# Kernel optimization log

Hardware: AMD Instinct MI355X
Metric: run time of the kernel (lower is better)

## Reference

```python
import jax, jax.numpy as jnp
import numpy as np


def setup_inputs() -> dict:
    key = jax.random.key(0)
    ks = jax.random.split(key, 7)
    T, B, X, H = 256, 64, 512, 2048
    s_ih = 1.0 / np.sqrt(H)
    return {
        "input": jax.random.normal(ks[0], (T, B, X), dtype=jnp.float32),
        "h_0": jax.random.normal(ks[1], (B, H), dtype=jnp.float32),
        "c_0": jax.random.normal(ks[2], (B, H), dtype=jnp.float32),
        "w_ih": jax.random.normal(ks[3], (4 * H, X), dtype=jnp.float32) * s_ih,
        "w_hh": jax.random.normal(ks[4], (4 * H, H), dtype=jnp.float32) * s_ih,
        "b_ih": jax.random.normal(ks[5], (4 * H,), dtype=jnp.float32) * s_ih,
        "b_hh": jax.random.normal(ks[6], (4 * H,), dtype=jnp.float32) * s_ih,
    }


def reference(input, h_0, c_0, w_ih, w_hh, b_ih, b_hh):
    H = h_0.shape[-1]
    # Precompute input projections for all timesteps in one big GEMM: [T,B,4H]
    x_proj = jnp.einsum("tbx,gx->tbg", input, w_ih) + b_ih + b_hh

    def step(carry, xg):
        h, c = carry
        gates = xg + h @ w_hh.T  # [B, 4H]
        i, f, g, o = jnp.split(gates, 4, axis=-1)  # torch LSTMCell gate order
        i = jax.nn.sigmoid(i)
        f = jax.nn.sigmoid(f)
        g = jnp.tanh(g)
        o = jax.nn.sigmoid(o)
        c_new = f * c + i * g
        h_new = o * jnp.tanh(c_new)
        y = jax.nn.softmax(h_new, axis=-1)  # per-step softmax over hidden dim
        return (h_new, c_new), y

    (h_T, c_T), ys = jax.lax.scan(step, (h_0, c_0), x_proj)
    return ys, h_T, c_T
```

## Files before the change

kernel.cpp:

```cpp
#include <hip/hip_runtime.h>

#define Tn 256
#define Bn 64
#define Xn 512
#define Hn 2048
#define Gn 8192
#define NWG 256

typedef short bf16x8 __attribute__((ext_vector_type(8)));
typedef float f32x4 __attribute__((ext_vector_type(4)));
typedef unsigned uint32x4 __attribute__((ext_vector_type(4)));

#define AL(p)    __hip_atomic_load((p), __ATOMIC_RELAXED, __HIP_MEMORY_SCOPE_AGENT)
#define AS(p, v) __hip_atomic_store((p), (v), __ATOMIC_RELAXED, __HIP_MEMORY_SCOPE_AGENT)

static __device__ __forceinline__ unsigned short f2bf(float f) {
    unsigned int u = __builtin_bit_cast(unsigned int, f);
    u += 0x7fffu + ((u >> 16) & 1u);
    return (unsigned short)(u >> 16);
}
static __device__ __forceinline__ float bf2f(unsigned short s) {
    unsigned int u = ((unsigned int)s) << 16;
    return __builtin_bit_cast(float, u);
}
static __device__ __forceinline__ void cvt4(const float* __restrict__ s,
                                            unsigned short* __restrict__ d, int i) {
    float4 v = ((const float4*)s)[i];
    ushort4 o;
    o.x = f2bf(v.x); o.y = f2bf(v.y); o.z = f2bf(v.z); o.w = f2bf(v.w);
    ((ushort4*)d)[i] = o;
}
static __device__ __forceinline__ float sigm(float x) {
    return 1.f / (1.f + __expf(-x));
}
static __device__ __forceinline__ float ftanh(float x) {
    float e = __expf(2.f * x);
    return (e - 1.f) / (e + 1.f);
}

template <int RING>
static __device__ __forceinline__ size_t hoff(int t) {
    if constexpr (RING) return (size_t)((t * 97) % 257) * 262144;
    else                return (size_t)(t & 1) * 262144;
}

template <int RING>
static __device__ __forceinline__ bf16x8 ldh(const unsigned short* p) {
    if constexpr (RING) {
        return *(const bf16x8*)p;
    } else {
        unsigned* q = (unsigned*)p;
        uint32x4 v;
        v[0] = AL(q + 0); v[1] = AL(q + 1); v[2] = AL(q + 2); v[3] = AL(q + 3);
        return __builtin_bit_cast(bf16x8, v);
    }
}
template <int RING>
static __device__ __forceinline__ float ldh1(const unsigned short* hb, int idx) {
    if constexpr (RING) {
        return bf2f(hb[idx]);
    } else {
        unsigned d = AL((unsigned*)(hb + (idx & ~1)));
        return bf2f((idx & 1) ? (unsigned short)(d >> 16) : (unsigned short)(d & 0xffffu));
    }
}

static __device__ __forceinline__ void flags_wait(unsigned* flags, unsigned t, int l) {
    if (!t) return;
    unsigned* p = flags + l * 4;
    for (;;) {
        unsigned a0 = AL(p + 0), a1 = AL(p + 1), a2 = AL(p + 2), a3 = AL(p + 3);
        bool ok = (a0 >= t) & (a1 >= t) & (a2 >= t) & (a3 >= t);
        if (__all(ok)) break;
        __builtin_amdgcn_s_sleep(1);
    }
}

__global__ void prologue3(const float* __restrict__ x, const float* __restrict__ h0,
                          const float* __restrict__ b_ih, const float* __restrict__ b_hh,
                          const float* __restrict__ w_ih,
                          unsigned short* __restrict__ Xb, unsigned short* __restrict__ XFrag,
                          unsigned short* __restrict__ hb0, float* __restrict__ bias,
                          unsigned* __restrict__ flags)
{
    int i = blockIdx.x * blockDim.x + threadIdx.x;
    const int n_x  = Tn * Bn * Xn / 4;
    const int n_xf = Gn * Xn / 4;
    const int n_h  = Bn * Hn / 4;
    const int n_b  = Gn / 4;
    if (i < n_x) { cvt4(x, Xb, i); return; }
    i -= n_x;
    if (i < n_xf) {
        int wg = i >> 12, r = i & 4095;
        int c = r >> 7, k = (r & 127) * 4;
        int g = c >> 3, u = c & 7;
        float4 v = *(const float4*)(w_ih + (size_t)(g * Hn + wg * 8 + u) * Xn + k);
        ushort4 o;
        o.x = f2bf(v.x); o.y = f2bf(v.y); o.z = f2bf(v.z); o.w = f2bf(v.w);
        int ct = c >> 4, kk = k >> 5, l = ((k >> 3) & 3) * 16 + (c & 15);
        *(ushort4*)((char*)XFrag + (size_t)wg * 32768 + (size_t)((ct * 16 + kk) * 64 + l) * 16 + (k & 7) * 2) = o;
        return;
    }
    i -= n_xf;
    if (i < n_h) {
        int flat = i * 4;
        int row = flat >> 11, unit0 = flat & 2047;
        float4 v = ((const float4*)h0)[i];
        ushort4 o;
        o.x = f2bf(v.x); o.y = f2bf(v.y); o.z = f2bf(v.z); o.w = f2bf(v.w);
        int dst = (((unit0 >> 3) << 6) + row) * 8 + (unit0 & 7);
        *(ushort4*)(hb0 + dst) = o;
        return;
    }
    i -= n_h;
    if (i < n_b) {
        float4 a = ((const float4*)b_ih)[i];
        float4 b = ((const float4*)b_hh)[i];
        ((float4*)bias)[i] = make_float4(a.x + b.x, a.y + b.y, a.z + b.z, a.w + b.w);
        return;
    }
    i -= n_b;
    if (i < 256) flags[i] = 0u;
}

#define MFMA2() \
    acc0 = __builtin_amdgcn_mfma_f32_16x16x32_bf16(a, b0, acc0, 0, 0, 0); \
    acc1 = __builtin_amdgcn_mfma_f32_16x16x32_bf16(a, b1, acc1, 0, 0, 0);

template <int RING>
__global__ __launch_bounds__(512, 1) void lstm_persist3(
    const unsigned short* __restrict__ Xb, const unsigned short* __restrict__ XFrag,
    const float* __restrict__ bias, const float* __restrict__ c0,
    char* __restrict__ hbase, const float* __restrict__ w_hh,
    float* __restrict__ ys, float* __restrict__ hT, float* __restrict__ cT,
    unsigned* __restrict__ flags)
{
    extern __shared__ char smem[];
    const unsigned short* LW = (const unsigned short*)smem;
    float* RED  = (float*)(smem + 131072);
    float* RED2 = (float*)(smem + 139264);

    const int wg  = blockIdx.x;
    const int tid = threadIdx.x;
    const int U0  = wg * 8;

    for (int i = tid; i < 32 * 512; i += 512) {
        int c = i >> 9, k = (i & 511) * 4;
        int g = c >> 3, u = c & 7;
        float4 v = *(const float4*)(w_hh + (size_t)(g * Hn + U0 + u) * Hn + k);
        ushort4 o;
        o.x = f2bf(v.x); o.y = f2bf(v.y); o.z = f2bf(v.z); o.w = f2bf(v.w);
        int ct = c >> 4, kk = k >> 5, l = ((k >> 3) & 3) * 16 + (c & 15);
        *(ushort4*)(smem + ((size_t)((ct * 64 + kk) * 64 + l) * 16 + (k & 7) * 2)) = o;
    }
    __syncthreads();

    const int w = tid >> 6, l = tid & 63;
    const int lm = l & 15, lh = l >> 4;
    const int kh = w >> 2, rblk = w & 3, rb = rblk * 16;
    const int kk0 = kh * 32;
    const int kx0 = kh * 8;

    const int u  = lm & 7;
    const bool hi = (lm & 8) != 0;
    const int r0g = rb + 4 * lh + (hi ? 2 : 0);

    float bi = 0.f, bf_ = 0.f, bg = 0.f, bo = 0.f, cs0 = 0.f, cs1 = 0.f;
    if (kh == 0) {
        bi  = bias[0 * Hn + U0 + u];
        bf_ = bias[1 * Hn + U0 + u];
        bg  = bias[2 * Hn + U0 + u];
        bo  = bias[3 * Hn + U0 + u];
        cs0 = c0[(size_t)r0g * Hn + U0 + u];
        cs1 = c0[(size_t)(r0g + 1) * Hn + U0 + u];
    }

    const char* xfb = (const char*)XFrag + (size_t)wg * 32768;

    for (int t = 0; t < Tn; ++t) {
        const unsigned short* hb = (const unsigned short*)(hbase + hoff<RING>(t));
        unsigned short* hn = (unsigned short*)(hbase + hoff<RING>(t + 1));

        f32x4 acc0 = {0.f, 0.f, 0.f, 0.f}, acc1 = {0.f, 0.f, 0.f, 0.f};

        {
            const unsigned short* xa = Xb + (size_t)(t * 64 + rb + lm) * Xn + lh * 8;
            bf16x8 aP[4];
            #pragma unroll
            for (int j = 0; j < 4; ++j) aP[j] = *(const bf16x8*)(xa + (kx0 + j) * 32);
            #pragma unroll 4
            for (int kkl = 0; kkl < 8; ++kkl) {
                bf16x8 a = aP[kkl & 3];
                if (kkl < 4) aP[kkl & 3] = *(const bf16x8*)(xa + (kx0 + kkl + 4) * 32);
                bf16x8 b0 = *(const bf16x8*)(xfb + ((size_t)((0 * 16 + kx0 + kkl) * 64 + l) << 4));
                bf16x8 b1 = *(const bf16x8*)(xfb + ((size_t)((1 * 16 + kx0 + kkl) * 64 + l) << 4));
                MFMA2();
            }
        }

        if (w == 0) flags_wait(flags, (unsigned)t, l);
        __syncthreads();

        {
            const unsigned short* ha = hb + (size_t)(rb + lm) * 8;
            bf16x8 aP[8];
            #pragma unroll
            for (int j = 0; j < 8; ++j)
                aP[j] = ldh<RING>(ha + (size_t)((kk0 + j) * 4 + lh) * 512);
            #pragma unroll 8
            for (int kkl = 0; kkl < 32; ++kkl) {
                bf16x8 a = aP[kkl & 7];
                if (kkl < 24)
                    aP[kkl & 7] = ldh<RING>(ha + (size_t)((kk0 + kkl + 8) * 4 + lh) * 512);
                bf16x8 b0 = *(const bf16x8*)(LW + ((size_t)((0 * 64 + kk0 + kkl) * 64 + l) << 3));
                bf16x8 b1 = *(const bf16x8*)(LW + ((size_t)((1 * 64 + kk0 + kkl) * 64 + l) << 3));
                MFMA2();
            }
        }

        const bool do_sm = (kh == 1) && (wg < Bn) && (t > 0);
        float sv[8];
        if (kh == 1) {
            int idx = (rblk * 64 + l) * 8;
            *(f32x4*)(RED + idx)     = acc0;
            *(f32x4*)(RED + idx + 4) = acc1;
            if (do_sm) {
                int row = wg;
                float m = -1e30f;
                #pragma unroll
                for (int j = 0; j < 8; ++j) {
                    int uu = rblk * 512 + j * 64 + l;
                    sv[j] = ldh1<RING>(hb, (uu >> 3) * 512 + row * 8 + (uu & 7));
                    m = fmaxf(m, sv[j]);
                }
                #pragma unroll
                for (int off = 32; off; off >>= 1) m = fmaxf(m, __shfl_xor(m, off));
                float s = 0.f;
                #pragma unroll
                for (int j = 0; j < 8; ++j) s += __expf(sv[j] - m);
                #pragma unroll
                for (int off = 32; off; off >>= 1) s += __shfl_xor(s, off);
                if (l == 0) { RED2[rblk * 2] = m; RED2[rblk * 2 + 1] = s; }
            }
        }
        __syncthreads();

        if (kh == 0) {
            int idx = (rblk * 64 + l) * 8;
            acc0 += *(const f32x4*)(RED + idx);
            acc1 += *(const f32x4*)(RED + idx + 4);
            f32x4 s0, s1;
            #pragma unroll
            for (int r = 0; r < 4; ++r) { s0[r] = __shfl_xor(acc0[r], 8); s1[r] = __shfl_xor(acc1[r], 8); }
            #pragma unroll
            for (int j = 0; j < 2; ++j) {
                int r = (hi ? 2 : 0) + j;
                float gi = (hi ? s0[r] : acc0[r]) + bi;
                float gf = (hi ? acc0[r] : s0[r]) + bf_;
                float gg = (hi ? s1[r] : acc1[r]) + bg;
                float go = (hi ? acc1[r] : s1[r]) + bo;
                float iv = sigm(gi), fv = sigm(gf), gv = ftanh(gg), ov = sigm(go);
                float cc = j ? cs1 : cs0;
                float cn = fv * cc + iv * gv;
                float hv = ov * ftanh(cn);
                if (j) cs1 = cn; else cs0 = cn;
                int rowg = r0g + j;
                unsigned short mybf = f2bf(hv);
                unsigned other = (unsigned)__shfl_xor((int)(unsigned)mybf, 1);
                if (!(u & 1)) {
                    unsigned pk = (unsigned)mybf | (other << 16);
                    AS((unsigned*)(hn + (size_t)wg * 512 + rowg * 8 + u), pk);
                }
                if (t == Tn - 1) {
                    size_t off = (size_t)rowg * Hn + U0 + u;
                    hT[off] = hv;
                    cT[off] = cn;
                }
            }
        }
        __syncthreads();
        if (tid == 0) AS(flags + wg, (unsigned)(t + 1));

        if (do_sm) {
            float m0 = RED2[0], sA = RED2[1], m1 = RED2[2], sB = RED2[3];
            float m2 = RED2[4], sC = RED2[5], m3 = RED2[6], sD = RED2[7];
            float gm = fmaxf(fmaxf(m0, m1), fmaxf(m2, m3));
            float gs = sA * __expf(m0 - gm) + sB * __expf(m1 - gm) +
                       sC * __expf(m2 - gm) + sD * __expf(m3 - gm);
            float inv = 1.f / gs;
            float* yr = ys + ((size_t)(t - 1) * Bn + wg) * Hn + rblk * 512;
            #pragma unroll
            for (int j = 0; j < 8; ++j) yr[j * 64 + l] = __expf(sv[j] - gm) * inv;
        }
    }

    if (w == 0) flags_wait(flags, (unsigned)Tn, l);
    __syncthreads();
    {
        const unsigned short* hfin = (const unsigned short*)(hbase + hoff<RING>(Tn));
        const bool act = (kh == 1) && (wg < Bn);
        float sv[8];
        if (act) {
            int row = wg;
            float m = -1e30f;
            #pragma unroll
            for (int j = 0; j < 8; ++j) {
                int uu = rblk * 512 + j * 64 + l;
                sv[j] = ldh1<RING>(hfin, (uu >> 3) * 512 + row * 8 + (uu & 7));
                m = fmaxf(m, sv[j]);
            }
            #pragma unroll
            for (int off = 32; off; off >>= 1) m = fmaxf(m, __shfl_xor(m, off));
            float s = 0.f;
            #pragma unroll
            for (int j = 0; j < 8; ++j) s += __expf(sv[j] - m);
            #pragma unroll
            for (int off = 32; off; off >>= 1) s += __shfl_xor(s, off);
            if (l == 0) { RED2[rblk * 2] = m; RED2[rblk * 2 + 1] = s; }
        }
        __syncthreads();
        if (act) {
            float m0 = RED2[0], sA = RED2[1], m1 = RED2[2], sB = RED2[3];
            float m2 = RED2[4], sC = RED2[5], m3 = RED2[6], sD = RED2[7];
            float gm = fmaxf(fmaxf(m0, m1), fmaxf(m2, m3));
            float gs = sA * __expf(m0 - gm) + sB * __expf(m1 - gm) +
                       sC * __expf(m2 - gm) + sD * __expf(m3 - gm);
            float inv = 1.f / gs;
            float* yr = ys + ((size_t)(Tn - 1) * Bn + wg) * Hn + rblk * 512;
            #pragma unroll
            for (int j = 0; j < 8; ++j) yr[j * 64 + l] = __expf(sv[j] - gm) * inv;
        }
    }
}

extern "C" void kernel_launch(void* const* d_in, const int* in_sizes, int n_in,
                              void* d_out, int out_size, void* d_ws, size_t ws_size,
                              hipStream_t stream) {
    const float* input = (const float*)d_in[0];
    const float* h0    = (const float*)d_in[1];
    const float* c0    = (const float*)d_in[2];
    const float* w_ih  = (const float*)d_in[3];
    const float* w_hh  = (const float*)d_in[4];
    const float* b_ih  = (const float*)d_in[5];
    const float* b_hh  = (const float*)d_in[6];

    float* ys = (float*)d_out;
    float* hT = ys + (size_t)Tn * Bn * Hn;
    float* cT = hT + (size_t)Bn * Hn;

    char* wsb = (char*)d_ws;
    unsigned short* Xb  = (unsigned short*)wsb;
    unsigned short* XF  = (unsigned short*)(wsb + 16777216);
    float* bias         = (float*)(wsb + 25165824);
    unsigned* flags     = (unsigned*)(wsb + 25198592);
    char* hbase         = wsb + 25199616;
    const size_t need_ring   = 25199616 + (size_t)257 * 262144;

    const int prol_items = Tn * Bn * Xn / 4 + Gn * Xn / 4 + Bn * Hn / 4 + Gn / 4 + 256;
    const int prol_blocks = (prol_items + 255) / 256;
    prologue3<<<dim3(prol_blocks), dim3(256), 0, stream>>>(
        input, h0, b_ih, b_hh, w_ih, Xb, XF, (unsigned short*)hbase, bias, flags);

    if (ws_size >= need_ring) {
        (void)hipFuncSetAttribute((const void*)lstm_persist3<1>,
                                  hipFuncAttributeMaxDynamicSharedMemorySize, 139328);
        lstm_persist3<1><<<dim3(NWG), dim3(512), 139328, stream>>>(
            Xb, XF, bias, c0, hbase, w_hh, ys, hT, cT, flags);
    } else {
        (void)hipFuncSetAttribute((const void*)lstm_persist3<0>,
                                  hipFuncAttributeMaxDynamicSharedMemorySize, 139328);
        lstm_persist3<0><<<dim3(NWG), dim3(512), 139328, stream>>>(
            Xb, XF, bias, c0, hbase, w_hh, ys, hT, cT, flags);
    }
}
```

Baseline: 2.131 ms.

## Shard grid barrier into atomic counters and widen per-wave row tiles

The per-workgroup flag array used as a grid barrier is replaced by 8 shard counters, one per 32 workgroups, incremented atomically. Each waiter now polls 8 words instead of 256. Work inside each workgroup is also regrouped: every wave computes two 16-row tiles over a quarter of K, so A and B fragments are reused across four MFMAs, and the cross-wave reduction goes through LDS in three partial stages. The cost is a larger reduction buffer and atomic contention on each shard.

Result: no change. 2.160 ms (+1.4%).

```diff
diff --git a/kernel.cpp b/kernel.cpp
--- a/kernel.cpp
+++ b/kernel.cpp
@@ -13,6 +13,7 @@
 
 #define AL(p)    __hip_atomic_load((p), __ATOMIC_RELAXED, __HIP_MEMORY_SCOPE_AGENT)
 #define AS(p, v) __hip_atomic_store((p), (v), __ATOMIC_RELAXED, __HIP_MEMORY_SCOPE_AGENT)
+#define AADD(p, v) __hip_atomic_fetch_add((p), (v), __ATOMIC_RELAXED, __HIP_MEMORY_SCOPE_AGENT)
 
 static __device__ __forceinline__ unsigned short f2bf(float f) {
     unsigned int u = __builtin_bit_cast(unsigned int, f);
@@ -43,7 +44,6 @@
     if constexpr (RING) return (size_t)((t * 97) % 257) * 262144;
     else                return (size_t)(t & 1) * 262144;
 }
-
 template <int RING>
 static __device__ __forceinline__ bf16x8 ldh(const unsigned short* p) {
     if constexpr (RING) {
@@ -65,13 +65,13 @@
     }
 }
 
-static __device__ __forceinline__ void flags_wait(unsigned* flags, unsigned t, int l) {
+static __device__ __forceinline__ void shards_wait(unsigned* sh, unsigned t, int l) {
     if (!t) return;
-    unsigned* p = flags + l * 4;
+    const unsigned target = t * 32u;
+    const bool mine = (l < 8);
     for (;;) {
-        unsigned a0 = AL(p + 0), a1 = AL(p + 1), a2 = AL(p + 2), a3 = AL(p + 3);
-        bool ok = (a0 >= t) & (a1 >= t) & (a2 >= t) & (a3 >= t);
-        if (__all(ok)) break;
+        unsigned a = mine ? AL(sh + l) : target;
+        if (__all(a >= target)) break;
         __builtin_amdgcn_s_sleep(1);
     }
 }
@@ -123,22 +123,24 @@
     if (i < 256) flags[i] = 0u;
 }
 
-#define MFMA2() \
-    acc0 = __builtin_amdgcn_mfma_f32_16x16x32_bf16(a, b0, acc0, 0, 0, 0); \
-    acc1 = __builtin_amdgcn_mfma_f32_16x16x32_bf16(a, b1, acc1, 0, 0, 0);
+#define MFMA4(a0v, a1v) \
+    acc00 = __builtin_amdgcn_mfma_f32_16x16x32_bf16((a0v), b0, acc00, 0, 0, 0); \
+    acc10 = __builtin_amdgcn_mfma_f32_16x16x32_bf16((a1v), b0, acc10, 0, 0, 0); \
+    acc01 = __builtin_amdgcn_mfma_f32_16x16x32_bf16((a0v), b1, acc01, 0, 0, 0); \
+    acc11 = __builtin_amdgcn_mfma_f32_16x16x32_bf16((a1v), b1, acc11, 0, 0, 0);
 
 template <int RING>
-__global__ __launch_bounds__(512, 1) void lstm_persist3(
+__global__ __launch_bounds__(512, 2) void lstm_persist4(
     const unsigned short* __restrict__ Xb, const unsigned short* __restrict__ XFrag,
     const float* __restrict__ bias, const float* __restrict__ c0,
     char* __restrict__ hbase, const float* __restrict__ w_hh,
     float* __restrict__ ys, float* __restrict__ hT, float* __restrict__ cT,
-    unsigned* __restrict__ flags)
+    unsigned* __restrict__ shards)
 {
     extern __shared__ char smem[];
     const unsigned short* LW = (const unsigned short*)smem;
     float* RED  = (float*)(smem + 131072);
-    float* RED2 = (float*)(smem + 139264);
+    float* RED2 = (float*)(smem + 155648);
 
     const int wg  = blockIdx.x;
     const int tid = threadIdx.x;
@@ -157,79 +159,94 @@
 
     const int w = tid >> 6, l = tid & 63;
     const int lm = l & 15, lh = l >> 4;
-    const int kh = w >> 2, rblk = w & 3, rb = rblk * 16;
-    const int kk0 = kh * 32;
-    const int kx0 = kh * 8;
+    const int kh = w >> 1, rblk = w & 1, rb = rblk * 32;
+    const int kk0 = kh * 16;
+    const int kx0 = kh * 4;
 
     const int u  = lm & 7;
     const bool hi = (lm & 8) != 0;
-    const int r0g = rb + 4 * lh + (hi ? 2 : 0);
-
-    float bi = 0.f, bf_ = 0.f, bg = 0.f, bo = 0.f, cs0 = 0.f, cs1 = 0.f;
+
+    float bi = 0.f, bf_ = 0.f, bg = 0.f, bo = 0.f;
+    float cs[2][2] = {{0.f, 0.f}, {0.f, 0.f}};
     if (kh == 0) {
         bi  = bias[0 * Hn + U0 + u];
         bf_ = bias[1 * Hn + U0 + u];
         bg  = bias[2 * Hn + U0 + u];
         bo  = bias[3 * Hn + U0 + u];
-        cs0 = c0[(size_t)r0g * Hn + U0 + u];
-        cs1 = c0[(size_t)(r0g + 1) * Hn + U0 + u];
+        #pragma unroll
+        for (int s = 0; s < 2; ++s)
+            #pragma unroll
+            for (int j = 0; j < 2; ++j)
+                cs[s][j] = c0[(size_t)(rb + s * 16 + 4 * lh + (hi ? 2 : 0) + j) * Hn + U0 + u];
     }
 
     const char* xfb = (const char*)XFrag + (size_t)wg * 32768;
+    const int srb = w - 2;
 
     for (int t = 0; t < Tn; ++t) {
         const unsigned short* hb = (const unsigned short*)(hbase + hoff<RING>(t));
         unsigned short* hn = (unsigned short*)(hbase + hoff<RING>(t + 1));
 
-        f32x4 acc0 = {0.f, 0.f, 0.f, 0.f}, acc1 = {0.f, 0.f, 0.f, 0.f};
+        f32x4 acc00 = {0,0,0,0}, acc01 = {0,0,0,0}, acc10 = {0,0,0,0}, acc11 = {0,0,0,0};
 
         {
-            const unsigned short* xa = Xb + (size_t)(t * 64 + rb + lm) * Xn + lh * 8;
-            bf16x8 aP[4];
-            #pragma unroll
-            for (int j = 0; j < 4; ++j) aP[j] = *(const bf16x8*)(xa + (kx0 + j) * 32);
-            #pragma unroll 4
-            for (int kkl = 0; kkl < 8; ++kkl) {
-                bf16x8 a = aP[kkl & 3];
-                if (kkl < 4) aP[kkl & 3] = *(const bf16x8*)(xa + (kx0 + kkl + 4) * 32);
+            const unsigned short* xa0 = Xb + (size_t)(t * 64 + rb + lm) * Xn + lh * 8;
+            const unsigned short* xa1 = xa0 + 16 * Xn;
+            bf16x8 xA0[4], xA1[4];
+            #pragma unroll
+            for (int j = 0; j < 4; ++j) {
+                xA0[j] = *(const bf16x8*)(xa0 + (kx0 + j) * 32);
+                xA1[j] = *(const bf16x8*)(xa1 + (kx0 + j) * 32);
+            }
+            #pragma unroll
+            for (int kkl = 0; kkl < 4; ++kkl) {
                 bf16x8 b0 = *(const bf16x8*)(xfb + ((size_t)((0 * 16 + kx0 + kkl) * 64 + l) << 4));
                 bf16x8 b1 = *(const bf16x8*)(xfb + ((size_t)((1 * 16 + kx0 + kkl) * 64 + l) << 4));
-                MFMA2();
-            }
-        }
-
-        if (w == 0) flags_wait(flags, (unsigned)t, l);
+                MFMA4(xA0[kkl], xA1[kkl]);
+            }
+        }
+
+        if (w == 0) shards_wait(shards, (unsigned)t, l);
         __syncthreads();
 
         {
-            const unsigned short* ha = hb + (size_t)(rb + lm) * 8;
-            bf16x8 aP[8];
-            #pragma unroll
-            for (int j = 0; j < 8; ++j)
-                aP[j] = ldh<RING>(ha + (size_t)((kk0 + j) * 4 + lh) * 512);
-            #pragma unroll 8
-            for (int kkl = 0; kkl < 32; ++kkl) {
-                bf16x8 a = aP[kkl & 7];
-                if (kkl < 24)
-                    aP[kkl & 7] = ldh<RING>(ha + (size_t)((kk0 + kkl + 8) * 4 + lh) * 512);
+            const unsigned short* ha0 = hb + (size_t)(rb + lm) * 8;
+            const unsigned short* ha1 = ha0 + 128;
+            bf16x8 aP0[4], aP1[4];
+            #pragma unroll
+            for (int j = 0; j < 4; ++j) {
+                int g = (kk0 + j) * 4 + lh;
+                aP0[j] = ldh<RING>(ha0 + (size_t)g * 512);
+                aP1[j] = ldh<RING>(ha1 + (size_t)g * 512);
+            }
+            #pragma unroll 4
+            for (int kkl = 0; kkl < 16; ++kkl) {
+                bf16x8 a0v = aP0[kkl & 3], a1v = aP1[kkl & 3];
+                if (kkl < 12) {
+                    int g = (kk0 + kkl + 4) * 4 + lh;
+                    aP0[kkl & 3] = ldh<RING>(ha0 + (size_t)g * 512);
+                    aP1[kkl & 3] = ldh<RING>(ha1 + (size_t)g * 512);
+                }
                 bf16x8 b0 = *(const bf16x8*)(LW + ((size_t)((0 * 64 + kk0 + kkl) * 64 + l) << 3));
                 bf16x8 b1 = *(const bf16x8*)(LW + ((size_t)((1 * 64 + kk0 + kkl) * 64 + l) << 3));
-                MFMA2();
-            }
-        }
-
-        const bool do_sm = (kh == 1) && (wg < Bn) && (t > 0);
+                MFMA4(a0v, a1v);
+            }
+        }
+
+        const bool do_sm = (srb >= 0 && srb < 4) && (wg < Bn) && (t > 0);
         float sv[8];
-        if (kh == 1) {
-            int idx = (rblk * 64 + l) * 8;
-            *(f32x4*)(RED + idx)     = acc0;
-            *(f32x4*)(RED + idx + 4) = acc1;
+        if (kh != 0) {
+            int idx = (((kh - 1) * 2 + rblk) * 64 + l) * 16;
+            *(f32x4*)(RED + idx + 0)  = acc00;
+            *(f32x4*)(RED + idx + 4)  = acc01;
+            *(f32x4*)(RED + idx + 8)  = acc10;
+            *(f32x4*)(RED + idx + 12) = acc11;
             if (do_sm) {
                 int row = wg;
                 float m = -1e30f;
                 #pragma unroll
                 for (int j = 0; j < 8; ++j) {
-                    int uu = rblk * 512 + j * 64 + l;
+                    int uu = srb * 512 + j * 64 + l;
                     sv[j] = ldh1<RING>(hb, (uu >> 3) * 512 + row * 8 + (uu & 7));
                     m = fmaxf(m, sv[j]);
                 }
@@ -240,72 +257,85 @@
                 for (int j = 0; j < 8; ++j) s += __expf(sv[j] - m);
                 #pragma unroll
                 for (int off = 32; off; off >>= 1) s += __shfl_xor(s, off);
-                if (l == 0) { RED2[rblk * 2] = m; RED2[rblk * 2 + 1] = s; }
+                if (l == 0) { RED2[srb * 2] = m; RED2[srb * 2 + 1] = s; }
             }
         }
         __syncthreads();
 
         if (kh == 0) {
-            int idx = (rblk * 64 + l) * 8;
-            acc0 += *(const f32x4*)(RED + idx);
-            acc1 += *(const f32x4*)(RED + idx + 4);
-            f32x4 s0, s1;
-            #pragma unroll
-            for (int r = 0; r < 4; ++r) { s0[r] = __shfl_xor(acc0[r], 8); s1[r] = __shfl_xor(acc1[r], 8); }
-            #pragma unroll
-            for (int j = 0; j < 2; ++j) {
-                int r = (hi ? 2 : 0) + j;
-                float gi = (hi ? s0[r] : acc0[r]) + bi;
-                float gf = (hi ? acc0[r] : s0[r]) + bf_;
-                float gg = (hi ? s1[r] : acc1[r]) + bg;
-                float go = (hi ? acc1[r] : s1[r]) + bo;
-                float iv = sigm(gi), fv = sigm(gf), gv = ftanh(gg), ov = sigm(go);
-                float cc = j ? cs1 : cs0;
-                float cn = fv * cc + iv * gv;
-                float hv = ov * ftanh(cn);
-                if (j) cs1 = cn; else cs0 = cn;
-                int rowg = r0g + j;
-                unsigned short mybf = f2bf(hv);
-                unsigned other = (unsigned)__shfl_xor((int)(unsigned)mybf, 1);
-                if (!(u & 1)) {
-                    unsigned pk = (unsigned)mybf | (other << 16);
-                    AS((unsigned*)(hn + (size_t)wg * 512 + rowg * 8 + u), pk);
+            #pragma unroll
+            for (int p = 0; p < 3; ++p) {
+                int idx = ((p * 2 + rblk) * 64 + l) * 16;
+                acc00 += *(const f32x4*)(RED + idx + 0);
+                acc01 += *(const f32x4*)(RED + idx + 4);
+                acc10 += *(const f32x4*)(RED + idx + 8);
+                acc11 += *(const f32x4*)(RED + idx + 12);
+            }
+            f32x4 sA[2], sB[2];
+            #pragma unroll
+            for (int r = 0; r < 4; ++r) {
+                sA[0][r] = __shfl_xor(acc00[r], 8); sB[0][r] = __shfl_xor(acc01[r], 8);
+                sA[1][r] = __shfl_xor(acc10[r], 8); sB[1][r] = __shfl_xor(acc11[r], 8);
+            }
+            #pragma unroll
+            for (int s = 0; s < 2; ++s) {
+                f32x4 aA = s ? acc10 : acc00;
+                f32x4 aB = s ? acc11 : acc01;
+                #pragma unroll
+                for (int j = 0; j < 2; ++j) {
+                    int r = (hi ? 2 : 0) + j;
+                    float gi = (hi ? sA[s][r] : aA[r]) + bi;
+                    float gf = (hi ? aA[r] : sA[s][r]) + bf_;
+                    float gg = (hi ? sB[s][r] : aB[r]) + bg;
+                    float go = (hi ? aB[r] : sB[s][r]) + bo;
+                    float iv = sigm(gi), fv = sigm(gf), gv = ftanh(gg), ov = sigm(go);
+                    float cc = cs[s][j];
+                    float cn = fv * cc + iv * gv;
+                    float hv = ov * ftanh(cn);
+                    cs[s][j] = cn;
+                    int rowg = rb + s * 16 + 4 * lh + (hi ? 2 : 0) + j;
+                    unsigned short mybf = f2bf(hv);
+                    unsigned other = (unsigned)__shfl_xor((int)(unsigned)mybf, 1);
+                    if (!(u & 1)) {
+                        AS((unsigned*)(hn + (size_t)wg * 512 + rowg * 8 + u),
+                           (unsigned)mybf | (other << 16));
+                    }
+                    if (t == Tn - 1) {
+                        size_t off = (size_t)rowg * Hn + U0 + u;
+                        hT[off] = hv;
+                        cT[off] = cn;
+                    }
                 }
-                if (t == Tn - 1) {
-                    size_t off = (size_t)rowg * Hn + U0 + u;
-                    hT[off] = hv;
-                    cT[off] = cn;
-                }
             }
         }
         __syncthreads();
-        if (tid == 0) AS(flags + wg, (unsigned)(t + 1));
+        if (tid == 0) AADD(shards + (wg >> 5), 1u);
 
         if (do_sm) {
-            float m0 = RED2[0], sA = RED2[1], m1 = RED2[2], sB = RED2[3];
-            float m2 = RED2[4], sC = RED2[5], m3 = RED2[6], sD = RED2[7];
+            float m0 = RED2[0], sA0 = RED2[1], m1 = RED2[2], sB0 = RED2[3];
+            float m2 = RED2[4], sC0 = RED2[5], m3 = RED2[6], sD0 = RED2[7];
             float gm = fmaxf(fmaxf(m0, m1), fmaxf(m2, m3));
-            float gs = sA * __expf(m0 - gm) + sB * __expf(m1 - gm) +
-                       sC * __expf(m2 - gm) + sD * __expf(m3 - gm);
+            float gs = sA0 * __expf(m0 - gm) + sB0 * __expf(m1 - gm) +
+                       sC0 * __expf(m2 - gm) + sD0 * __expf(m3 - gm);
             float inv = 1.f / gs;
-            float* yr = ys + ((size_t)(t - 1) * Bn + wg) * Hn + rblk * 512;
+            float* yr = ys + ((size_t)(t - 1) * Bn + wg) * Hn + srb * 512;
             #pragma unroll
             for (int j = 0; j < 8; ++j) yr[j * 64 + l] = __expf(sv[j] - gm) * inv;
         }
     }
 
-    if (w == 0) flags_wait(flags, (unsigned)Tn, l);
+    if (w == 0) shards_wait(shards, (unsigned)Tn, l);
     __syncthreads();
     {
         const unsigned short* hfin = (const unsigned short*)(hbase + hoff<RING>(Tn));
-        const bool act = (kh == 1) && (wg < Bn);
+        const bool act = (srb >= 0 && srb < 4) && (wg < Bn);
         float sv[8];
         if (act) {
             int row = wg;
             float m = -1e30f;
             #pragma unroll
             for (int j = 0; j < 8; ++j) {
-                int uu = rblk * 512 + j * 64 + l;
+                int uu = srb * 512 + j * 64 + l;
                 sv[j] = ldh1<RING>(hfin, (uu >> 3) * 512 + row * 8 + (uu & 7));
                 m = fmaxf(m, sv[j]);
             }
@@ -316,17 +346,17 @@
             for (int j = 0; j < 8; ++j) s += __expf(sv[j] - m);
             #pragma unroll
             for (int off = 32; off; off >>= 1) s += __shfl_xor(s, off);
-            if (l == 0) { RED2[rblk * 2] = m; RED2[rblk * 2 + 1] = s; }
+            if (l == 0) { RED2[srb * 2] = m; RED2[srb * 2 + 1] = s; }
         }
         __syncthreads();
         if (act) {
-            float m0 = RED2[0], sA = RED2[1], m1 = RED2[2], sB = RED2[3];
-            float m2 = RED2[4], sC = RED2[5], m3 = RED2[6], sD = RED2[7];
+            float m0 = RED2[0], sA0 = RED2[1], m1 = RED2[2], sB0 = RED2[3];
+            float m2 = RED2[4], sC0 = RED2[5], m3 = RED2[6], sD0 = RED2[7];
             float gm = fmaxf(fmaxf(m0, m1), fmaxf(m2, m3));
-            float gs = sA * __expf(m0 - gm) + sB * __expf(m1 - gm) +
-                       sC * __expf(m2 - gm) + sD * __expf(m3 - gm);
+            float gs = sA0 * __expf(m0 - gm) + sB0 * __expf(m1 - gm) +
+                       sC0 * __expf(m2 - gm) + sD0 * __expf(m3 - gm);
             float inv = 1.f / gs;
-            float* yr = ys + ((size_t)(Tn - 1) * Bn + wg) * Hn + rblk * 512;
+            float* yr = ys + ((size_t)(Tn - 1) * Bn + wg) * Hn + srb * 512;
             #pragma unroll
             for (int j = 0; j < 8; ++j) yr[j * 64 + l] = __expf(sv[j] - gm) * inv;
         }
@@ -354,7 +384,7 @@
     float* bias         = (float*)(wsb + 25165824);
     unsigned* flags     = (unsigned*)(wsb + 25198592);
     char* hbase         = wsb + 25199616;
-    const size_t need_ring   = 25199616 + (size_t)257 * 262144;
+    const size_t need_ring = 25199616 + (size_t)257 * 262144;
 
     const int prol_items = Tn * Bn * Xn / 4 + Gn * Xn / 4 + Bn * Hn / 4 + Gn / 4 + 256;
     const int prol_blocks = (prol_items + 255) / 256;
@@ -362,14 +392,14 @@
         input, h0, b_ih, b_hh, w_ih, Xb, XF, (unsigned short*)hbase, bias, flags);
 
     if (ws_size >= need_ring) {
-        (void)hipFuncSetAttribute((const void*)lstm_persist3<1>,
-                                  hipFuncAttributeMaxDynamicSharedMemorySize, 139328);
-        lstm_persist3<1><<<dim3(NWG), dim3(512), 139328, stream>>>(
+        (void)hipFuncSetAttribute((const void*)lstm_persist4<1>,
+                                  hipFuncAttributeMaxDynamicSharedMemorySize, 155680);
+        lstm_persist4<1><<<dim3(NWG), dim3(512), 155680, stream>>>(
             Xb, XF, bias, c0, hbase, w_hh, ys, hT, cT, flags);
     } else {
-        (void)hipFuncSetAttribute((const void*)lstm_persist3<0>,
-                                  hipFuncAttributeMaxDynamicSharedMemorySize, 139328);
-        lstm_persist3<0><<<dim3(NWG), dim3(512), 139328, stream>>>(
+        (void)hipFuncSetAttribute((const void*)lstm_persist4<0>,
+                                  hipFuncAttributeMaxDynamicSharedMemorySize, 155680);
+        lstm_persist4<0><<<dim3(NWG), dim3(512), 155680, stream>>>(
             Xb, XF, bias, c0, hbase, w_hh, ys, hT, cT, flags);
     }
 }
```

## Replace global flag barrier with per-row-quarter counters and single-K-split waves

Applied to the files above, without the earlier changes.

Each workgroup drops from 8 to 4 waves. Each wave now covers the full K range for its 16 batch rows, so the shared-memory K-split reduction and its block barriers go away. The global per-workgroup flag wait is replaced by per-row-quarter atomic counters, so each wave waits only for the producers of the h rows it reads. The softmax owner is rotated across workgroups by timestep, and the h ring buffer is shrunk to 129 slots. The intent is to cut synchronisation latency on the recurrent critical path, at the cost of half as many waves to hide MFMA and memory latency.

After: 3.125 ms. 1.47x slower.

```diff
diff --git a/kernel.cpp b/kernel.cpp
--- a/kernel.cpp
+++ b/kernel.cpp
@@ -13,6 +13,7 @@
 
 #define AL(p)    __hip_atomic_load((p), __ATOMIC_RELAXED, __HIP_MEMORY_SCOPE_AGENT)
 #define AS(p, v) __hip_atomic_store((p), (v), __ATOMIC_RELAXED, __HIP_MEMORY_SCOPE_AGENT)
+#define AADD(p, v) __hip_atomic_fetch_add((p), (v), __ATOMIC_RELAXED, __HIP_MEMORY_SCOPE_AGENT)
 
 static __device__ __forceinline__ unsigned short f2bf(float f) {
     unsigned int u = __builtin_bit_cast(unsigned int, f);
@@ -40,10 +41,9 @@
 
 template <int RING>
 static __device__ __forceinline__ size_t hoff(int t) {
-    if constexpr (RING) return (size_t)((t * 97) % 257) * 262144;
+    if constexpr (RING) return (size_t)((t * 67) % 129) * 262144;
     else                return (size_t)(t & 1) * 262144;
 }
-
 template <int RING>
 static __device__ __forceinline__ bf16x8 ldh(const unsigned short* p) {
     if constexpr (RING) {
@@ -65,18 +65,17 @@
     }
 }
 
-static __device__ __forceinline__ void flags_wait(unsigned* flags, unsigned t, int l) {
-    if (!t) return;
-    unsigned* p = flags + l * 4;
+static __device__ __forceinline__ void quarter_wait(const unsigned* qf, unsigned target, int l) {
+    if (!target) return;
+    const unsigned* p = qf + (l & 31) * 16;
     for (;;) {
-        unsigned a0 = AL(p + 0), a1 = AL(p + 1), a2 = AL(p + 2), a3 = AL(p + 3);
-        bool ok = (a0 >= t) & (a1 >= t) & (a2 >= t) & (a3 >= t);
-        if (__all(ok)) break;
+        unsigned a = (l < 32) ? AL(p) : target;
+        if (__all(a >= target)) break;
         __builtin_amdgcn_s_sleep(1);
     }
 }
 
-__global__ void prologue3(const float* __restrict__ x, const float* __restrict__ h0,
+__global__ void prologue4(const float* __restrict__ x, const float* __restrict__ h0,
                           const float* __restrict__ b_ih, const float* __restrict__ b_hh,
                           const float* __restrict__ w_ih,
                           unsigned short* __restrict__ Xb, unsigned short* __restrict__ XFrag,
@@ -120,15 +119,11 @@
         return;
     }
     i -= n_b;
-    if (i < 256) flags[i] = 0u;
-}
-
-#define MFMA2() \
-    acc0 = __builtin_amdgcn_mfma_f32_16x16x32_bf16(a, b0, acc0, 0, 0, 0); \
-    acc1 = __builtin_amdgcn_mfma_f32_16x16x32_bf16(a, b1, acc1, 0, 0, 0);
+    if (i < 2048) flags[i] = 0u;
+}
 
 template <int RING>
-__global__ __launch_bounds__(512, 1) void lstm_persist3(
+__global__ __launch_bounds__(256, 1) void lstm_persist8(
     const unsigned short* __restrict__ Xb, const unsigned short* __restrict__ XFrag,
     const float* __restrict__ bias, const float* __restrict__ c0,
     char* __restrict__ hbase, const float* __restrict__ w_hh,
@@ -137,14 +132,13 @@
 {
     extern __shared__ char smem[];
     const unsigned short* LW = (const unsigned short*)smem;
-    float* RED  = (float*)(smem + 131072);
-    float* RED2 = (float*)(smem + 139264);
+    float* RED2 = (float*)(smem + 131072);
 
     const int wg  = blockIdx.x;
     const int tid = threadIdx.x;
     const int U0  = wg * 8;
 
-    for (int i = tid; i < 32 * 512; i += 512) {
+    for (int i = tid; i < 32 * 512; i += 256) {
         int c = i >> 9, k = (i & 511) * 4;
         int g = c >> 3, u = c & 7;
         float4 v = *(const float4*)(w_hh + (size_t)(g * Hn + U0 + u) * Hn + k);
@@ -157,98 +151,66 @@
 
     const int w = tid >> 6, l = tid & 63;
     const int lm = l & 15, lh = l >> 4;
-    const int kh = w >> 2, rblk = w & 3, rb = rblk * 16;
-    const int kk0 = kh * 32;
-    const int kx0 = kh * 8;
+    const int R0 = w * 16;
 
     const int u  = lm & 7;
     const bool hi = (lm & 8) != 0;
-    const int r0g = rb + 4 * lh + (hi ? 2 : 0);
-
-    float bi = 0.f, bf_ = 0.f, bg = 0.f, bo = 0.f, cs0 = 0.f, cs1 = 0.f;
-    if (kh == 0) {
-        bi  = bias[0 * Hn + U0 + u];
-        bf_ = bias[1 * Hn + U0 + u];
-        bg  = bias[2 * Hn + U0 + u];
-        bo  = bias[3 * Hn + U0 + u];
-        cs0 = c0[(size_t)r0g * Hn + U0 + u];
-        cs1 = c0[(size_t)(r0g + 1) * Hn + U0 + u];
-    }
+    const int r0g = R0 + 4 * lh + (hi ? 2 : 0);
+
+    const float bi  = bias[0 * Hn + U0 + u];
+    const float bf_ = bias[1 * Hn + U0 + u];
+    const float bg  = bias[2 * Hn + U0 + u];
+    const float bo  = bias[3 * Hn + U0 + u];
+    float cs0 = c0[(size_t)r0g * Hn + U0 + u];
+    float cs1 = c0[(size_t)(r0g + 1) * Hn + U0 + u];
 
     const char* xfb = (const char*)XFrag + (size_t)wg * 32768;
+    const unsigned* qf = flags + w * 32 * 16;
+    unsigned* pubp = flags + (w * 32 + (wg >> 3)) * 16;
 
     for (int t = 0; t < Tn; ++t) {
         const unsigned short* hb = (const unsigned short*)(hbase + hoff<RING>(t));
         unsigned short* hn = (unsigned short*)(hbase + hoff<RING>(t + 1));
 
-        f32x4 acc0 = {0.f, 0.f, 0.f, 0.f}, acc1 = {0.f, 0.f, 0.f, 0.f};
+        f32x4 acc0 = {0,0,0,0}, acc1 = {0,0,0,0};
 
         {
-            const unsigned short* xa = Xb + (size_t)(t * 64 + rb + lm) * Xn + lh * 8;
-            bf16x8 aP[4];
-            #pragma unroll
-            for (int j = 0; j < 4; ++j) aP[j] = *(const bf16x8*)(xa + (kx0 + j) * 32);
+            const unsigned short* xa = Xb + (size_t)(t * 64 + R0 + lm) * Xn + lh * 8;
+            bf16x8 xA[4];
+            #pragma unroll
+            for (int j = 0; j < 4; ++j) xA[j] = *(const bf16x8*)(xa + j * 32);
             #pragma unroll 4
-            for (int kkl = 0; kkl < 8; ++kkl) {
-                bf16x8 a = aP[kkl & 3];
-                if (kkl < 4) aP[kkl & 3] = *(const bf16x8*)(xa + (kx0 + kkl + 4) * 32);
-                bf16x8 b0 = *(const bf16x8*)(xfb + ((size_t)((0 * 16 + kx0 + kkl) * 64 + l) << 4));
-                bf16x8 b1 = *(const bf16x8*)(xfb + ((size_t)((1 * 16 + kx0 + kkl) * 64 + l) << 4));
-                MFMA2();
-            }
-        }
-
-        if (w == 0) flags_wait(flags, (unsigned)t, l);
-        __syncthreads();
+            for (int kk = 0; kk < 16; ++kk) {
+                bf16x8 a = xA[kk & 3];
+                if (kk < 12) xA[kk & 3] = *(const bf16x8*)(xa + (kk + 4) * 32);
+                bf16x8 b0 = *(const bf16x8*)(xfb + ((size_t)((0 * 16 + kk) * 64 + l) << 4));
+                bf16x8 b1 = *(const bf16x8*)(xfb + ((size_t)((1 * 16 + kk) * 64 + l) << 4));
+                acc0 = __builtin_amdgcn_mfma_f32_16x16x32_bf16(a, b0, acc0, 0, 0, 0);
+                acc1 = __builtin_amdgcn_mfma_f32_16x16x32_bf16(a, b1, acc1, 0, 0, 0);
+            }
+        }
+
+        quarter_wait(qf, (unsigned)t * 8u, l);
 
         {
-            const unsigned short* ha = hb + (size_t)(rb + lm) * 8;
+            const unsigned short* ha = hb + (size_t)(R0 + lm) * 8;
             bf16x8 aP[8];
             #pragma unroll
             for (int j = 0; j < 8; ++j)
-                aP[j] = ldh<RING>(ha + (size_t)((kk0 + j) * 4 + lh) * 512);
+                aP[j] = ldh<RING>(ha + (size_t)(j * 4 + lh) * 512);
             #pragma unroll 8
-            for (int kkl = 0; kkl < 32; ++kkl) {
-                bf16x8 a = aP[kkl & 7];
-                if (kkl < 24)
-                    aP[kkl & 7] = ldh<RING>(ha + (size_t)((kk0 + kkl + 8) * 4 + lh) * 512);
-                bf16x8 b0 = *(const bf16x8*)(LW + ((size_t)((0 * 64 + kk0 + kkl) * 64 + l) << 3));
-                bf16x8 b1 = *(const bf16x8*)(LW + ((size_t)((1 * 64 + kk0 + kkl) * 64 + l) << 3));
-                MFMA2();
-            }
-        }
-
-        const bool do_sm = (kh == 1) && (wg < Bn) && (t > 0);
-        float sv[8];
-        if (kh == 1) {
-            int idx = (rblk * 64 + l) * 8;
-            *(f32x4*)(RED + idx)     = acc0;
-            *(f32x4*)(RED + idx + 4) = acc1;
-            if (do_sm) {
-                int row = wg;
-                float m = -1e30f;
-                #pragma unroll
-                for (int j = 0; j < 8; ++j) {
-                    int uu = rblk * 512 + j * 64 + l;
-                    sv[j] = ldh1<RING>(hb, (uu >> 3) * 512 + row * 8 + (uu & 7));
-                    m = fmaxf(m, sv[j]);
-                }
-                #pragma unroll
-                for (int off = 32; off; off >>= 1) m = fmaxf(m, __shfl_xor(m, off));
-                float s = 0.f;
-                #pragma unroll
-                for (int j = 0; j < 8; ++j) s += __expf(sv[j] - m);
-                #pragma unroll
-                for (int off = 32; off; off >>= 1) s += __shfl_xor(s, off);
-                if (l == 0) { RED2[rblk * 2] = m; RED2[rblk * 2 + 1] = s; }
-            }
-        }
-        __syncthreads();
-
-        if (kh == 0) {
-            int idx = (rblk * 64 + l) * 8;
-            acc0 += *(const f32x4*)(RED + idx);
-            acc1 += *(const f32x4*)(RED + idx + 4);
+            for (int kk = 0; kk < 64; ++kk) {
+                bf16x8 a = aP[kk & 7];
+                if (kk < 56)
+                    aP[kk & 7] = ldh<RING>(ha + (size_t)((kk + 8) * 4 + lh) * 512);
+                bf16x8 b0 = *(const bf16x8*)(LW + ((size_t)((0 * 64 + kk) * 64 + l) << 3));
+                bf16x8 b1 = *(const bf16x8*)(LW + ((size_t)((1 * 64 + kk) * 64 + l) << 3));
+                acc0 = __builtin_amdgcn_mfma_f32_16x16x32_bf16(a, b0, acc0, 0, 0, 0);
+                acc1 = __builtin_amdgcn_mfma_f32_16x16x32_bf16(a, b1, acc1, 0, 0, 0);
+            }
+        }
+
+        {
             f32x4 s0, s1;
             #pragma unroll
             for (int r = 0; r < 4; ++r) { s0[r] = __shfl_xor(acc0[r], 8); s1[r] = __shfl_xor(acc1[r], 8); }
@@ -268,8 +230,8 @@
                 unsigned short mybf = f2bf(hv);
                 unsigned other = (unsigned)__shfl_xor((int)(unsigned)mybf, 1);
                 if (!(u & 1)) {
-                    unsigned pk = (unsigned)mybf | (other << 16);
-                    AS((unsigned*)(hn + (size_t)wg * 512 + rowg * 8 + u), pk);
+                    AS((unsigned*)(hn + (size_t)wg * 512 + rowg * 8 + u),
+                       (unsigned)mybf | (other << 16));
                 }
                 if (t == Tn - 1) {
                     size_t off = (size_t)rowg * Hn + U0 + u;
@@ -278,45 +240,74 @@
                 }
             }
         }
-        __syncthreads();
-        if (tid == 0) AS(flags + wg, (unsigned)(t + 1));
-
-        if (do_sm) {
+        asm volatile("s_waitcnt vmcnt(0)" ::: "memory");
+
+        const int srow = wg - (t & 3) * 64;
+        const bool sm = (srow >= 0) && (srow < Bn) && (t > 0);
+
+        if (RING || !sm) {
+            if (l == 0) AADD(pubp, 1u);
+        }
+
+        float sv[8];
+        if (sm) {
+            quarter_wait(flags + (srow >> 4) * 32 * 16, (unsigned)t * 8u, l);
+            float pm = -1e30f;
+            #pragma unroll
+            for (int j = 0; j < 8; ++j) {
+                int uu = w * 512 + j * 64 + l;
+                sv[j] = ldh1<RING>(hb, (uu >> 3) * 512 + srow * 8 + (uu & 7));
+                pm = fmaxf(pm, sv[j]);
+            }
+            #pragma unroll
+            for (int off = 32; off; off >>= 1) pm = fmaxf(pm, __shfl_xor(pm, off));
+            float ps = 0.f;
+            #pragma unroll
+            for (int j = 0; j < 8; ++j) ps += __expf(sv[j] - pm);
+            #pragma unroll
+            for (int off = 32; off; off >>= 1) ps += __shfl_xor(ps, off);
+            if (l == 0) { RED2[w * 2] = pm; RED2[w * 2 + 1] = ps; }
+        }
+        if (sm) __syncthreads();
+        if constexpr (!RING) {
+            if (sm && l == 0) AADD(pubp, 1u);
+        }
+        if (sm) {
             float m0 = RED2[0], sA = RED2[1], m1 = RED2[2], sB = RED2[3];
             float m2 = RED2[4], sC = RED2[5], m3 = RED2[6], sD = RED2[7];
             float gm = fmaxf(fmaxf(m0, m1), fmaxf(m2, m3));
             float gs = sA * __expf(m0 - gm) + sB * __expf(m1 - gm) +
                        sC * __expf(m2 - gm) + sD * __expf(m3 - gm);
             float inv = 1.f / gs;
-            float* yr = ys + ((size_t)(t - 1) * Bn + wg) * Hn + rblk * 512;
+            float* yr = ys + ((size_t)(t - 1) * Bn + srow) * Hn + w * 512;
             #pragma unroll
             for (int j = 0; j < 8; ++j) yr[j * 64 + l] = __expf(sv[j] - gm) * inv;
-        }
-    }
-
-    if (w == 0) flags_wait(flags, (unsigned)Tn, l);
-    __syncthreads();
+            __syncthreads();
+        }
+    }
+
     {
         const unsigned short* hfin = (const unsigned short*)(hbase + hoff<RING>(Tn));
-        const bool act = (kh == 1) && (wg < Bn);
+        const int srow = wg;
+        const bool act = (srow < Bn);
         float sv[8];
         if (act) {
-            int row = wg;
-            float m = -1e30f;
+            quarter_wait(flags + (srow >> 4) * 32 * 16, (unsigned)Tn * 8u, l);
+            float pm = -1e30f;
             #pragma unroll
             for (int j = 0; j < 8; ++j) {
-                int uu = rblk * 512 + j * 64 + l;
-                sv[j] = ldh1<RING>(hfin, (uu >> 3) * 512 + row * 8 + (uu & 7));
-                m = fmaxf(m, sv[j]);
-            }
-            #pragma unroll
-            for (int off = 32; off; off >>= 1) m = fmaxf(m, __shfl_xor(m, off));
-            float s = 0.f;
-            #pragma unroll
-            for (int j = 0; j < 8; ++j) s += __expf(sv[j] - m);
-            #pragma unroll
-            for (int off = 32; off; off >>= 1) s += __shfl_xor(s, off);
-            if (l == 0) { RED2[rblk * 2] = m; RED2[rblk * 2 + 1] = s; }
+                int uu = w * 512 + j * 64 + l;
+                sv[j] = ldh1<RING>(hfin, (uu >> 3) * 512 + srow * 8 + (uu & 7));
+                pm = fmaxf(pm, sv[j]);
+            }
+            #pragma unroll
+            for (int off = 32; off; off >>= 1) pm = fmaxf(pm, __shfl_xor(pm, off));
+            float ps = 0.f;
+            #pragma unroll
+            for (int j = 0; j < 8; ++j) ps += __expf(sv[j] - pm);
+            #pragma unroll
+            for (int off = 32; off; off >>= 1) ps += __shfl_xor(ps, off);
+            if (l == 0) { RED2[w * 2] = pm; RED2[w * 2 + 1] = ps; }
         }
         __syncthreads();
         if (act) {
@@ -326,7 +317,7 @@
             float gs = sA * __expf(m0 - gm) + sB * __expf(m1 - gm) +
                        sC * __expf(m2 - gm) + sD * __expf(m3 - gm);
             float inv = 1.f / gs;
-            float* yr = ys + ((size_t)(Tn - 1) * Bn + wg) * Hn + rblk * 512;
+            float* yr = ys + ((size_t)(Tn - 1) * Bn + srow) * Hn + w * 512;
             #pragma unroll
             for (int j = 0; j < 8; ++j) yr[j * 64 + l] = __expf(sv[j] - gm) * inv;
         }
@@ -353,23 +344,23 @@
     unsigned short* XF  = (unsigned short*)(wsb + 16777216);
     float* bias         = (float*)(wsb + 25165824);
     unsigned* flags     = (unsigned*)(wsb + 25198592);
-    char* hbase         = wsb + 25199616;
-    const size_t need_ring   = 25199616 + (size_t)257 * 262144;
-
-    const int prol_items = Tn * Bn * Xn / 4 + Gn * Xn / 4 + Bn * Hn / 4 + Gn / 4 + 256;
+    char* hbase         = wsb + 25206784;
+    const size_t need_ring = 25206784 + (size_t)129 * 262144;
+
+    const int prol_items = Tn * Bn * Xn / 4 + Gn * Xn / 4 + Bn * Hn / 4 + Gn / 4 + 2048;
     const int prol_blocks = (prol_items + 255) / 256;
-    prologue3<<<dim3(prol_blocks), dim3(256), 0, stream>>>(
+    prologue4<<<dim3(prol_blocks), dim3(256), 0, stream>>>(
         input, h0, b_ih, b_hh, w_ih, Xb, XF, (unsigned short*)hbase, bias, flags);
 
     if (ws_size >= need_ring) {
-        (void)hipFuncSetAttribute((const void*)lstm_persist3<1>,
-                                  hipFuncAttributeMaxDynamicSharedMemorySize, 139328);
-        lstm_persist3<1><<<dim3(NWG), dim3(512), 139328, stream>>>(
+        (void)hipFuncSetAttribute((const void*)lstm_persist8<1>,
+                                  hipFuncAttributeMaxDynamicSharedMemorySize, 131136);
+        lstm_persist8<1><<<dim3(NWG), dim3(256), 131136, stream>>>(
             Xb, XF, bias, c0, hbase, w_hh, ys, hT, cT, flags);
     } else {
-        (void)hipFuncSetAttribute((const void*)lstm_persist3<0>,
-                                  hipFuncAttributeMaxDynamicSharedMemorySize, 139328);
-        lstm_persist3<0><<<dim3(NWG), dim3(512), 139328, stream>>>(
+        (void)hipFuncSetAttribute((const void*)lstm_persist8<0>,
+                                  hipFuncAttributeMaxDynamicSharedMemorySize, 131136);
+        lstm_persist8<0><<<dim3(NWG), dim3(256), 131136, stream>>>(
             Xb, XF, bias, c0, hbase, w_hh, ys, hT, cT, flags);
     }
 }
```
